# Kernel optimization log

Hardware: AMD Instinct MI355X
Metric: run time of the kernel (lower is better)

Reference implementation:

```python
import jax, jax.numpy as jnp
import numpy as np

N_NODES = 100000
N_EDGES = 1600000
NODE_DIM = 128
EDGE_DIM = 64
MSG_DIM = 128
NODE_DIM_OUT = 128


def setup_inputs() -> dict:
    key = jax.random.key(0)
    k1, k2, k3, k4, k5, k6, k7 = jax.random.split(key, 7)
    node_emb = jax.random.normal(k1, (N_NODES, NODE_DIM), dtype=jnp.float32)
    edge_index = jax.random.randint(k2, (2, N_EDGES), 0, N_NODES, dtype=jnp.int64)
    edge_emb = jax.random.normal(k3, (N_EDGES, EDGE_DIM), dtype=jnp.float32)
    # Linear params (stored as [in, out]; torch uses [out, in] with x @ W.T)
    s_msg = 1.0 / np.sqrt(NODE_DIM + EDGE_DIM)
    W_msg = jax.random.uniform(k4, (NODE_DIM + EDGE_DIM, MSG_DIM), jnp.float32, -s_msg, s_msg)
    b_msg = jax.random.uniform(k5, (MSG_DIM,), jnp.float32, -s_msg, s_msg)
    s_upd = 1.0 / np.sqrt(NODE_DIM + MSG_DIM)
    W_upd = jax.random.uniform(k6, (NODE_DIM + MSG_DIM, NODE_DIM_OUT), jnp.float32, -s_upd, s_upd)
    b_upd = jax.random.uniform(k7, (NODE_DIM_OUT,), jnp.float32, -s_upd, s_upd)
    return {"node_emb": node_emb, "edge_index": edge_index, "edge_emb": edge_emb,
            "W_msg": W_msg, "b_msg": b_msg, "W_upd": W_upd, "b_upd": b_upd}


def reference(node_emb, edge_index, edge_emb, W_msg, b_msg, W_upd, b_upd):
    # PyG MessagePassing default flow: x_j = x[edge_index[0]] (source),
    # messages aggregated (mean) at edge_index[1] (target).
    src = edge_index[0]
    dst = edge_index[1]
    n = node_emb.shape[0]

    x_j = node_emb[src]                                    # [E, node_dim] gather
    msg_in = jnp.concatenate([x_j, edge_emb], axis=1)      # [E, node_dim+edge_dim]
    msg = jax.nn.relu(msg_in @ W_msg + b_msg)              # [E, msg_dim]

    # scatter-mean aggregate to nodes
    summed = jax.ops.segment_sum(msg, dst, num_segments=n)  # [N, msg_dim]
    counts = jax.ops.segment_sum(jnp.ones((msg.shape[0],), dtype=msg.dtype), dst, num_segments=n)
    mean_msg = summed / jnp.maximum(counts, 1.0)[:, None]

    upd_in = jnp.concatenate([node_emb, mean_msg], axis=1)  # [N, node_dim+msg_dim]
    h = jax.nn.relu(upd_in @ W_upd + b_upd)                 # [N, node_dim_out]
    # dropout is identity in eval mode; normalize=False (default)
    return h
```

## Files before the change

kernel.cpp:

```cpp
#include <hip/hip_runtime.h>
#include <hip/hip_bf16.h>

#define N_NODES 100000
#define N_EDGES 1600000
#define D_NODE 128
#define D_EDGE 64
#define D_MSG 128
#define K1 192
#define K2 256
#define D_OUT 128
#define NSB 98
#define TILE 64
#define NT (N_EDGES / TILE)

using frag8 = __attribute__((ext_vector_type(8))) short;
using facc  = __attribute__((ext_vector_type(4))) float;

static __device__ __forceinline__ unsigned short f2bf(float f) {
    unsigned int u = __float_as_uint(f);
    u = u + 0x7fffu + ((u >> 16) & 1u);
    return (unsigned short)(u >> 16);
}
static __device__ __forceinline__ float bflo(unsigned int u) { return __uint_as_float(u << 16); }
static __device__ __forceinline__ float bfhi(unsigned int u) { return __uint_as_float(u & 0xffff0000u); }

union F8 { unsigned short s[8]; frag8 f; uint4 u4; };

static __device__ __forceinline__ frag8 pack8(float4 a, float4 b) {
    F8 u;
    u.s[0] = f2bf(a.x); u.s[1] = f2bf(a.y); u.s[2] = f2bf(a.z); u.s[3] = f2bf(a.w);
    u.s[4] = f2bf(b.x); u.s[5] = f2bf(b.y); u.s[6] = f2bf(b.z); u.s[7] = f2bf(b.w);
    return u.f;
}

__global__ void prep_w_kernel(const float* __restrict__ Wm, const float* __restrict__ Wu,
                              unsigned short* __restrict__ WtM, unsigned short* __restrict__ WtU) {
    int idx0 = blockIdx.x * blockDim.x + threadIdx.x;
    int stride = gridDim.x * blockDim.x;
    for (int idx = idx0; idx < 128 * K1; idx += stride) {
        int o = idx / K1, k = idx - o * K1;
        WtM[idx] = f2bf(Wm[k * D_MSG + o]);
    }
    for (int idx = idx0; idx < 128 * K2; idx += stride) {
        int o = idx >> 8, k = idx & 255;
        WtU[idx] = f2bf(Wu[k * D_OUT + o]);
    }
}

__global__ void prep_node_kernel(const float* __restrict__ node_emb,
                                 unsigned int* __restrict__ nodeB32) {
    int idx0 = blockIdx.x * blockDim.x + threadIdx.x;
    int stride = gridDim.x * blockDim.x;
    const int total = N_NODES * 64;
    for (int i = idx0; i < total; i += stride) {
        float2 v = *(const float2*)&node_emb[(size_t)i * 2];
        nodeB32[i] = (unsigned)f2bf(v.x) | ((unsigned)f2bf(v.y) << 16);
    }
}

__global__ void hist_kernel(const int* __restrict__ dst, int* __restrict__ cnt) {
    int idx0 = blockIdx.x * blockDim.x + threadIdx.x;
    int stride = gridDim.x * blockDim.x;
    for (int e = idx0; e < N_EDGES; e += stride) {
        int d = min(max(dst[e], 0), N_NODES - 1);
        atomicAdd(&cnt[d], 1);
    }
}

__global__ __launch_bounds__(1024) void scan_blocks(const int* __restrict__ cnt,
                                                    int* __restrict__ base,
                                                    int* __restrict__ part) {
    __shared__ int sh[1024];
    int i = blockIdx.x * 1024 + threadIdx.x;
    int c = (i < N_NODES) ? cnt[i] : 0;
    sh[threadIdx.x] = c;
    __syncthreads();
    for (int s = 1; s < 1024; s <<= 1) {
        int t = (threadIdx.x >= s) ? sh[threadIdx.x - s] : 0;
        __syncthreads();
        sh[threadIdx.x] += t;
        __syncthreads();
    }
    if (i < N_NODES) base[i] = sh[threadIdx.x] - c;
    if (threadIdx.x == 1023) part[blockIdx.x] = sh[1023];
}

__global__ __launch_bounds__(128) void scan_partials(int* __restrict__ part) {
    __shared__ int sh[128];
    int i = threadIdx.x;
    int c = (i < NSB) ? part[i] : 0;
    sh[i] = c;
    __syncthreads();
    for (int s = 1; s < 128; s <<= 1) {
        int t = (i >= s) ? sh[i - s] : 0;
        __syncthreads();
        sh[i] += t;
        __syncthreads();
    }
    if (i < NSB) part[i] = sh[i] - c;
}

__global__ __launch_bounds__(1024) void scan_add(int* __restrict__ base, const int* __restrict__ part) {
    int i = blockIdx.x * 1024 + threadIdx.x;
    if (i < N_NODES) base[i] += part[blockIdx.x];
}

__global__ void scatter_kernel(const int* __restrict__ dst, const int* __restrict__ src,
                               const int* __restrict__ base, int* __restrict__ cursor,
                               int* __restrict__ perm, int* __restrict__ srcS,
                               int* __restrict__ dstS) {
    int idx0 = blockIdx.x * blockDim.x + threadIdx.x;
    int stride = gridDim.x * blockDim.x;
    for (int e = idx0; e < N_EDGES; e += stride) {
        int d = min(max(dst[e], 0), N_NODES - 1);
        int pos = base[d] + atomicAdd(&cursor[d], 1);
        perm[pos] = e;
        srcS[pos] = src[e];
        dstS[pos] = d;
    }
}

__global__ __launch_bounds__(256, 3) void msg_fused_kernel(
    const unsigned short* __restrict__ nodeB, const int* __restrict__ srcS,
    const int* __restrict__ perm, const int* __restrict__ dstS,
    const float* __restrict__ edge_emb, const unsigned short* __restrict__ WtM,
    const float* __restrict__ b_msg, const int* __restrict__ base,
    const int* __restrict__ cnt, float* __restrict__ mean)
{
    __shared__ unsigned short sIn[TILE][192];
    __shared__ unsigned short sMsg[TILE][128];

    const int lane = threadIdx.x & 63;
    const int wav  = threadIdx.x >> 6;
    const int j = lane & 15;
    const int q = lane >> 4;

    frag8 wfr[2][6];
#pragma unroll
    for (int m2 = 0; m2 < 2; ++m2) {
        const unsigned short* wrow = WtM + ((wav * 2 + m2) * 16 + j) * K1;
#pragma unroll
        for (int kc = 0; kc < 6; ++kc)
            wfr[m2][kc] = *(const frag8*)&wrow[(kc * 4 + q) * 8];
    }
    float bias[2][4];
#pragma unroll
    for (int m2 = 0; m2 < 2; ++m2)
#pragma unroll
        for (int r = 0; r < 4; ++r) bias[m2][r] = b_msg[(wav * 2 + m2) * 16 + q * 4 + r];

    const int eL = threadIdx.x >> 2;
    const int qt = threadIdx.x & 3;
    const int swz = eL & 7;

    uint4  nst[4];
    float4 est[4];

    const int t0 = blockIdx.x;

    {
        const int e = t0 * TILE + eL;
        const int sp = min(max(srcS[e], 0), N_NODES - 1);
        const unsigned short* nrow = nodeB + (size_t)sp * D_NODE + qt * 32;
#pragma unroll
        for (int i = 0; i < 4; ++i) nst[i] = *(const uint4*)&nrow[i * 8];
        const float* erow = edge_emb + (size_t)perm[e] * D_EDGE + qt * 16;
#pragma unroll
        for (int i = 0; i < 4; ++i) est[i] = *(const float4*)&erow[i * 4];
    }

#pragma unroll 1
    for (int t = t0; t < NT; t += gridDim.x) {
        const int e0 = t * TILE;

        __syncthreads();

        {
            unsigned short* drow = &sIn[eL][0];
#pragma unroll
            for (int i = 0; i < 4; ++i)
                *(uint4*)&drow[((4 * qt + i) ^ swz) * 8] = nst[i];
#pragma unroll
            for (int h = 0; h < 2; ++h) {
                F8 u;
                u.f = pack8(est[h * 2], est[h * 2 + 1]);
                *(uint4*)&drow[((16 + 2 * qt + h) ^ swz) * 8] = u.u4;
            }
        }
        __syncthreads();

        const int tn = t + gridDim.x;
        if (tn < NT) {
            const int e = tn * TILE + eL;
            const int sp = min(max(srcS[e], 0), N_NODES - 1);
            const unsigned short* nrow = nodeB + (size_t)sp * D_NODE + qt * 32;
#pragma unroll
            for (int i = 0; i < 4; ++i) nst[i] = *(const uint4*)&nrow[i * 8];
            const float* erow = edge_emb + (size_t)perm[e] * D_EDGE + qt * 16;
#pragma unroll
            for (int i = 0; i < 4; ++i) est[i] = *(const float4*)&erow[i * 4];
        }

        facc acc[2][4];
#pragma unroll
        for (int m2 = 0; m2 < 2; ++m2)
#pragma unroll
            for (int eg = 0; eg < 4; ++eg) { facc z = {0.f,0.f,0.f,0.f}; acc[m2][eg] = z; }

        const int rsw = j & 7;
#pragma unroll
        for (int eg = 0; eg < 4; ++eg) {
            const unsigned short* irow = &sIn[eg * 16 + j][0];
#pragma unroll
            for (int kc = 0; kc < 6; ++kc) {
                frag8 b = *(const frag8*)&irow[((4 * kc + q) ^ rsw) * 8];
                acc[0][eg] = __builtin_amdgcn_mfma_f32_16x16x32_bf16(wfr[0][kc], b, acc[0][eg], 0, 0, 0);
                acc[1][eg] = __builtin_amdgcn_mfma_f32_16x16x32_bf16(wfr[1][kc], b, acc[1][eg], 0, 0, 0);
            }
        }

#pragma unroll
        for (int eg = 0; eg < 4; ++eg) {
            unsigned short* mrow = &sMsg[eg * 16 + j][0];
#pragma unroll
            for (int m2 = 0; m2 < 2; ++m2) {
                float v0 = fmaxf(acc[m2][eg][0] + bias[m2][0], 0.f);
                float v1 = fmaxf(acc[m2][eg][1] + bias[m2][1], 0.f);
                float v2 = fmaxf(acc[m2][eg][2] + bias[m2][2], 0.f);
                float v3 = fmaxf(acc[m2][eg][3] + bias[m2][3], 0.f);
                uint2 w;
                w.x = (unsigned)f2bf(v0) | ((unsigned)f2bf(v1) << 16);
                w.y = (unsigned)f2bf(v2) | ((unsigned)f2bf(v3) << 16);
                int c64 = wav * 8 + m2 * 4 + q;
                *(uint2*)&mrow[(c64 ^ rsw) * 4] = w;
            }
        }
        __syncthreads();

        const int d_lo = dstS[e0];
        const int d_hi = dstS[e0 + TILE - 1];
        for (int n = d_lo + wav; n <= d_hi; n += 4) {
            const int b = base[n];
            const int c = cnt[n];
            const int lo = max(b - e0, 0);
            const int hi = min(b + c - e0, TILE);
            float s0 = 0.f, s1 = 0.f;
            for (int r = lo; r < hi; ++r) {
                const unsigned* mr = (const unsigned*)&sMsg[r][0];
                unsigned u = mr[(((lane >> 1) ^ (r & 7)) << 1) | (lane & 1)];
                s0 += bflo(u); s1 += bfhi(u);
            }
            const float inv = 1.0f / fmaxf((float)c, 1.0f);
            s0 *= inv; s1 *= inv;
            float* mp = mean + (size_t)n * D_MSG + lane * 2;
            if (b >= e0 && b + c <= e0 + TILE) {
                *(float2*)mp = make_float2(s0, s1);
            } else {
                atomicAdd(mp + 0, s0);
                atomicAdd(mp + 1, s1);
            }
        }
    }
}

__global__ __launch_bounds__(256) void node_gemm_kernel(
    const unsigned short* __restrict__ nodeB, const float* __restrict__ mean,
    const unsigned short* __restrict__ WtU, const float* __restrict__ b_upd,
    float* __restrict__ out)
{
    __shared__ unsigned short sW[128 * K2];

    for (int idx = threadIdx.x; idx < 128 * 32; idx += 256) {
        int o = idx >> 5, ch = idx & 31;
        *(uint4*)&sW[o * K2 + (ch ^ (o & 7)) * 8] = *(const uint4*)&WtU[o * K2 + ch * 8];
    }

    const int lane = threadIdx.x & 63;
    const int wav  = threadIdx.x >> 6;
    const int j = lane & 15;
    const int q = lane >> 4;
    const int rs = j & 7;

    float bias[32];
#pragma unroll
    for (int mt = 0; mt < 8; ++mt)
#pragma unroll
        for (int r = 0; r < 4; ++r) bias[mt * 4 + r] = b_upd[mt * 16 + q * 4 + r];
    __syncthreads();

    const int n0w = blockIdx.x * 256 + wav * 64;

#pragma unroll 1
    for (int g = 0; g < 4; ++g) {
        const int n = n0w + g * 16 + j;
        const bool valid = (n < N_NODES);
        const size_t nn = valid ? (size_t)n : 0;

        frag8 bfr[8];
        const unsigned short* nrow = nodeB + nn * D_NODE;
#pragma unroll
        for (int kc = 0; kc < 4; ++kc)
            bfr[kc] = *(const frag8*)&nrow[kc * 32 + q * 8];
        const float* mrow = mean + nn * D_MSG;
#pragma unroll
        for (int kc = 0; kc < 4; ++kc) {
            float4 a = *(const float4*)&mrow[kc * 32 + q * 8];
            float4 c = *(const float4*)&mrow[kc * 32 + q * 8 + 4];
            bfr[4 + kc] = pack8(a, c);
        }

        facc acc[8];
#pragma unroll
        for (int mt = 0; mt < 8; ++mt) { facc z = {0.f, 0.f, 0.f, 0.f}; acc[mt] = z; }

#pragma unroll
        for (int mt = 0; mt < 8; ++mt) {
            const unsigned short* wrow = &sW[(mt * 16 + j) * K2];
#pragma unroll
            for (int kc = 0; kc < 8; ++kc) {
                frag8 a = *(const frag8*)&wrow[((kc * 4 + q) ^ rs) * 8];
                acc[mt] = __builtin_amdgcn_mfma_f32_16x16x32_bf16(a, bfr[kc], acc[mt], 0, 0, 0);
            }
        }

        if (valid) {
            float* orow = out + (size_t)n * D_OUT;
#pragma unroll
            for (int mt = 0; mt < 8; ++mt)
#pragma unroll
                for (int r = 0; r < 4; ++r)
                    orow[mt * 16 + q * 4 + r] = fmaxf(acc[mt][r] + bias[mt * 4 + r], 0.f);
        }
    }
}

__global__ __launch_bounds__(256) void msg_agg_kernel_fb(
    const float* __restrict__ node_emb, const int* __restrict__ src,
    const float* __restrict__ edge_emb, const unsigned short* __restrict__ WtM,
    const float* __restrict__ b_msg, const int* __restrict__ perm,
    const int* __restrict__ dstS, const int* __restrict__ cnt,
    float* __restrict__ mean)
{
    __shared__ unsigned short sW[128 * K1];

    for (int idx = threadIdx.x; idx < 128 * 24; idx += 256) {
        int o = idx / 24, ch = idx % 24;
        *(uint4*)&sW[o * K1 + (ch ^ (o & 7)) * 8] = *(const uint4*)&WtM[o * K1 + ch * 8];
    }

    const int lane = threadIdx.x & 63;
    const int wav  = threadIdx.x >> 6;
    const int j = lane & 15;
    const int q = lane >> 4;

    float bias[32];
#pragma unroll
    for (int mt = 0; mt < 8; ++mt)
#pragma unroll
        for (int r = 0; r < 4; ++r) bias[mt * 4 + r] = b_msg[mt * 16 + q * 4 + r];
    __syncthreads();

    const int e0w = blockIdx.x * 256 + wav * 64;
    float carry[32];
    int carry_d = -1;

#pragma unroll 1
    for (int g = 0; g < 4; ++g) {
        const int e = e0w + g * 16 + j;
        const int p = perm[e];
        const int d = dstS[e];
        const int sp = min(max(src[p], 0), N_NODES - 1);
        const float invc = 1.0f / (float)cnt[d];

        frag8 bfr[6];
        const float* nrow = node_emb + (size_t)sp * D_NODE;
#pragma unroll
        for (int kc = 0; kc < 4; ++kc) {
            float4 a = *(const float4*)&nrow[kc * 32 + q * 8];
            float4 c = *(const float4*)&nrow[kc * 32 + q * 8 + 4];
            bfr[kc] = pack8(a, c);
        }
        const float* erow = edge_emb + (size_t)p * D_EDGE;
#pragma unroll
        for (int kc = 0; kc < 2; ++kc) {
            float4 a = *(const float4*)&erow[kc * 32 + q * 8];
            float4 c = *(const float4*)&erow[kc * 32 + q * 8 + 4];
            bfr[4 + kc] = pack8(a, c);
        }

        facc acc[8];
#pragma unroll
        for (int mt = 0; mt < 8; ++mt) { facc z = {0.f, 0.f, 0.f, 0.f}; acc[mt] = z; }

#pragma unroll
        for (int mt = 0; mt < 8; ++mt) {
            const unsigned short* wrow = &sW[(mt * 16 + j) * K1];
            const int rs = j & 7;
#pragma unroll
            for (int kc = 0; kc < 6; ++kc) {
                frag8 a = *(const frag8*)&wrow[((kc * 4 + q) ^ rs) * 8];
                acc[mt] = __builtin_amdgcn_mfma_f32_16x16x32_bf16(a, bfr[kc], acc[mt], 0, 0, 0);
            }
        }

        float v[32];
#pragma unroll
        for (int mt = 0; mt < 8; ++mt)
#pragma unroll
            for (int r = 0; r < 4; ++r) {
                float t = acc[mt][r] + bias[mt * 4 + r];
                v[mt * 4 + r] = fmaxf(t, 0.f) * invc;
            }

        int dprev = __shfl_up(d, 1, 16);
        int head = (j == 0 || d != dprev) ? 1 : 0;
        int seg = head;
#pragma unroll
        for (int s = 1; s < 16; s <<= 1) { int t = __shfl_up(seg, s, 16); if (j >= s) seg += t; }
        int sg1 = __shfl_up(seg, 1, 16);
        int sg2 = __shfl_up(seg, 2, 16);
        int sg4 = __shfl_up(seg, 4, 16);
        int sg8 = __shfl_up(seg, 8, 16);
        bool ok1 = (j >= 1) && (sg1 == seg);
        bool ok2 = (j >= 2) && (sg2 == seg);
        bool ok4 = (j >= 4) && (sg4 == seg);
        bool ok8 = (j >= 8) && (sg8 == seg);

#pragma unroll
        for (int i = 0; i < 32; ++i) { float t = __shfl_up(v[i], 1, 16); if (ok1) v[i] += t; }
#pragma unroll
        for (int i = 0; i < 32; ++i) { float t = __shfl_up(v[i], 2, 16); if (ok2) v[i] += t; }
#pragma unroll
        for (int i = 0; i < 32; ++i) { float t = __shfl_up(v[i], 4, 16); if (ok4) v[i] += t; }
#pragma unroll
        for (int i = 0; i < 32; ++i) { float t = __shfl_up(v[i], 8, 16); if (ok8) v[i] += t; }

        int d0 = __shfl(d, 0, 16);
        if (g > 0) {
            if (d0 != carry_d) {
                if (j == 0) {
                    float* mrow = mean + (size_t)carry_d * D_MSG;
#pragma unroll
                    for (int mt = 0; mt < 8; ++mt)
#pragma unroll
                        for (int r = 0; r < 4; ++r)
                            atomicAdd(&mrow[mt * 16 + q * 4 + r], carry[mt * 4 + r]);
                }
            } else if (seg == 1) {
#pragma unroll
                for (int i = 0; i < 32; ++i) v[i] += carry[i];
            }
        }

#pragma unroll
        for (int i = 0; i < 32; ++i) carry[i] = __shfl(v[i], 15, 16);
        carry_d = __shfl(d, 15, 16);

        int dnext = __shfl_down(d, 1, 16);
        bool tail = (j < 15) ? (dnext != d) : (g == 3);
        if (tail) {
            float* mrow = mean + (size_t)d * D_MSG;
#pragma unroll
            for (int mt = 0; mt < 8; ++mt)
#pragma unroll
                for (int r = 0; r < 4; ++r)
                    atomicAdd(&mrow[mt * 16 + q * 4 + r], v[mt * 4 + r]);
        }
    }
}

__global__ __launch_bounds__(256) void node_kernel_fb(
    const float* __restrict__ node_emb, const float* __restrict__ mean,
    const unsigned short* __restrict__ WtU, const float* __restrict__ b_upd,
    float* __restrict__ out)
{
    __shared__ unsigned short sW[128 * K2];

    for (int idx = threadIdx.x; idx < 128 * 32; idx += 256) {
        int o = idx >> 5, ch = idx & 31;
        *(uint4*)&sW[o * K2 + (ch ^ (o & 7)) * 8] = *(const uint4*)&WtU[o * K2 + ch * 8];
    }

    const int lane = threadIdx.x & 63;
    const int wav  = threadIdx.x >> 6;
    const int j = lane & 15;
    const int q = lane >> 4;

    float bias[32];
#pragma unroll
    for (int mt = 0; mt < 8; ++mt)
#pragma unroll
        for (int r = 0; r < 4; ++r) bias[mt * 4 + r] = b_upd[mt * 16 + q * 4 + r];
    __syncthreads();

    const int n0w = blockIdx.x * 256 + wav * 64;

#pragma unroll 1
    for (int g = 0; g < 4; ++g) {
        const int n = n0w + g * 16 + j;
        const bool valid = (n < N_NODES);
        const size_t nn = valid ? (size_t)n : 0;

        frag8 bfr[8];
        const float* nrow = node_emb + nn * D_NODE;
#pragma unroll
        for (int kc = 0; kc < 4; ++kc) {
            float4 a = *(const float4*)&nrow[kc * 32 + q * 8];
            float4 c = *(const float4*)&nrow[kc * 32 + q * 8 + 4];
            bfr[kc] = pack8(a, c);
        }
        const float* mrow = mean + nn * D_MSG;
#pragma unroll
        for (int kc = 0; kc < 4; ++kc) {
            float4 a = *(const float4*)&mrow[kc * 32 + q * 8];
            float4 c = *(const float4*)&mrow[kc * 32 + q * 8 + 4];
            bfr[4 + kc] = pack8(a, c);
        }

        facc acc[8];
#pragma unroll
        for (int mt = 0; mt < 8; ++mt) { facc z = {0.f, 0.f, 0.f, 0.f}; acc[mt] = z; }

#pragma unroll
        for (int mt = 0; mt < 8; ++mt) {
            const unsigned short* wrow = &sW[(mt * 16 + j) * K2];
            const int rs = j & 7;
#pragma unroll
            for (int kc = 0; kc < 8; ++kc) {
                frag8 a = *(const frag8*)&wrow[((kc * 4 + q) ^ rs) * 8];
                acc[mt] = __builtin_amdgcn_mfma_f32_16x16x32_bf16(a, bfr[kc], acc[mt], 0, 0, 0);
            }
        }

        if (valid) {
            float* orow = out + (size_t)n * D_OUT;
#pragma unroll
            for (int mt = 0; mt < 8; ++mt)
#pragma unroll
                for (int r = 0; r < 4; ++r)
                    orow[mt * 16 + q * 4 + r] = fmaxf(acc[mt][r] + bias[mt * 4 + r], 0.f);
        }
    }
}

extern "C" void kernel_launch(void* const* d_in, const int* in_sizes, int n_in,
                              void* d_out, int out_size, void* d_ws, size_t ws_size,
                              hipStream_t stream) {
    const float* node_emb = (const float*)d_in[0];
    const int*   edge_idx = (const int*)d_in[1];
    const float* edge_emb = (const float*)d_in[2];
    const float* W_msg    = (const float*)d_in[3];
    const float* b_msg    = (const float*)d_in[4];
    const float* W_upd    = (const float*)d_in[5];
    const float* b_upd    = (const float*)d_in[6];
    float* out = (float*)d_out;

    const int* src = edge_idx;
    const int* dst = edge_idx + N_EDGES;

    char* W = (char*)d_ws;

    if (ws_size >= 97315200ULL) {
        float* mean  = (float*)(W + 0);
        int* cnt     = (int*)(W + 51200000);
        int* cursor  = (int*)(W + 51600000);
        int* base    = (int*)(W + 52000000);
        int* part    = (int*)(W + 52400000);
        int* perm    = (int*)(W + 52400512);
        int* srcS    = (int*)(W + 58800512);
        int* dstS    = (int*)(W + 65200512);
        unsigned short* WtM   = (unsigned short*)(W + 71600512);
        unsigned short* WtU   = (unsigned short*)(W + 71649664);
        unsigned short* nodeB = (unsigned short*)(W + 71715200);

        hipMemsetAsync(d_ws, 0, 52000000, stream);

        prep_w_kernel<<<224, 256, 0, stream>>>(W_msg, W_upd, WtM, WtU);
        prep_node_kernel<<<2048, 256, 0, stream>>>(node_emb, (unsigned int*)nodeB);
        hist_kernel<<<1024, 256, 0, stream>>>(dst, cnt);
        scan_blocks<<<NSB, 1024, 0, stream>>>(cnt, base, part);
        scan_partials<<<1, 128, 0, stream>>>(part);
        scan_add<<<NSB, 1024, 0, stream>>>(base, part);
        scatter_kernel<<<1024, 256, 0, stream>>>(dst, src, base, cursor, perm, srcS, dstS);
        msg_fused_kernel<<<2048, 256, 0, stream>>>(nodeB, srcS, perm, dstS, edge_emb,
                                                   WtM, b_msg, base, cnt, mean);
        node_gemm_kernel<<<391, 256, 0, stream>>>(nodeB, mean, WtU, b_upd, out);
    } else {
        float* mean  = (float*)W;
        int* cnt     = (int*)(W + 51200000);
        int* cursor  = (int*)(W + 51600000);
        int* base    = (int*)(W + 52000000);
        int* part    = (int*)(W + 52400000);
        int* perm    = (int*)(W + 52400512);
        int* dstS    = (int*)(W + 58800512);
        int* srcS    = (int*)(W + 65200512);
        unsigned short* WtM = (unsigned short*)(W + 71600512);
        unsigned short* WtU = (unsigned short*)(W + 71649664);

        hipMemsetAsync(d_ws, 0, 52000000, stream);

        prep_w_kernel<<<224, 256, 0, stream>>>(W_msg, W_upd, WtM, WtU);
        hist_kernel<<<1024, 256, 0, stream>>>(dst, cnt);
        scan_blocks<<<NSB, 1024, 0, stream>>>(cnt, base, part);
        scan_partials<<<1, 128, 0, stream>>>(part);
        scan_add<<<NSB, 1024, 0, stream>>>(base, part);
        scatter_kernel<<<1024, 256, 0, stream>>>(dst, src, base, cursor, perm, srcS, dstS);
        msg_agg_kernel_fb<<<6250, 256, 0, stream>>>(node_emb, src, edge_emb, WtM,
                                                    b_msg, perm, dstS, cnt, mean);
        node_kernel_fb<<<391, 256, 0, stream>>>(node_emb, mean, WtU, b_upd, out);
    }
}
```

Before: 604.9 us.

## Pre-sort edge embeddings to bf16, replace boundary atomics with spill+cleanup pass

The scatter pass now writes edge embeddings converted to bf16 in destination-sorted order, so the message kernel reads them contiguously at half the size instead of gathering fp32 rows through perm. Partial sums for nodes that straddle tile boundaries go to a per-tile spill buffer, and a new cleanup kernel reduces them into mean instead of using float atomics. This lets the large memset of mean be dropped. The weight, node-conversion and histogram prep kernels are merged into one launch, and the message kernel's occupancy hint rises from 3 to 4. In exchange the scatter pass writes roughly 200MB more, and the workspace requirement grows a lot, so a smaller workspace falls back to the slower path.

```diff
diff --git a/kernel.cpp b/kernel.cpp
--- a/kernel.cpp
+++ b/kernel.cpp
@@ -33,8 +33,10 @@
     return u.f;
 }
 
-__global__ void prep_w_kernel(const float* __restrict__ Wm, const float* __restrict__ Wu,
-                              unsigned short* __restrict__ WtM, unsigned short* __restrict__ WtU) {
+__global__ void prep_all_kernel(const float* __restrict__ Wm, const float* __restrict__ Wu,
+                                const float* __restrict__ node_emb, const int* __restrict__ dst,
+                                unsigned short* __restrict__ WtM, unsigned short* __restrict__ WtU,
+                                unsigned int* __restrict__ nodeB32, int* __restrict__ cnt) {
     int idx0 = blockIdx.x * blockDim.x + threadIdx.x;
     int stride = gridDim.x * blockDim.x;
     for (int idx = idx0; idx < 128 * K1; idx += stride) {
@@ -45,22 +47,11 @@
         int o = idx >> 8, k = idx & 255;
         WtU[idx] = f2bf(Wu[k * D_OUT + o]);
     }
-}
-
-__global__ void prep_node_kernel(const float* __restrict__ node_emb,
-                                 unsigned int* __restrict__ nodeB32) {
-    int idx0 = blockIdx.x * blockDim.x + threadIdx.x;
-    int stride = gridDim.x * blockDim.x;
     const int total = N_NODES * 64;
     for (int i = idx0; i < total; i += stride) {
         float2 v = *(const float2*)&node_emb[(size_t)i * 2];
         nodeB32[i] = (unsigned)f2bf(v.x) | ((unsigned)f2bf(v.y) << 16);
     }
-}
-
-__global__ void hist_kernel(const int* __restrict__ dst, int* __restrict__ cnt) {
-    int idx0 = blockIdx.x * blockDim.x + threadIdx.x;
-    int stride = gridDim.x * blockDim.x;
     for (int e = idx0; e < N_EDGES; e += stride) {
         int d = min(max(dst[e], 0), N_NODES - 1);
         atomicAdd(&cnt[d], 1);
@@ -105,6 +96,290 @@
     if (i < N_NODES) base[i] += part[blockIdx.x];
 }
 
+__global__ void scatter2_kernel(const int* __restrict__ dst, const int* __restrict__ src,
+                                const float* __restrict__ edge_emb,
+                                const int* __restrict__ base, int* __restrict__ cursor,
+                                int* __restrict__ srcS, int* __restrict__ dstS,
+                                unsigned short* __restrict__ edgeB) {
+    int idx0 = blockIdx.x * blockDim.x + threadIdx.x;
+    int stride = gridDim.x * blockDim.x;
+    for (int e = idx0; e < N_EDGES; e += stride) {
+        int d = min(max(dst[e], 0), N_NODES - 1);
+        int pos = base[d] + atomicAdd(&cursor[d], 1);
+        srcS[pos] = src[e];
+        dstS[pos] = d;
+        const float* er = edge_emb + (size_t)e * D_EDGE;
+        unsigned short* ob = edgeB + (size_t)pos * D_EDGE;
+#pragma unroll
+        for (int c = 0; c < 4; ++c) {
+            float4 a = *(const float4*)&er[c * 16 + 0];
+            float4 b = *(const float4*)&er[c * 16 + 4];
+            float4 g = *(const float4*)&er[c * 16 + 8];
+            float4 h = *(const float4*)&er[c * 16 + 12];
+            F8 u0; u0.f = pack8(a, b);
+            F8 u1; u1.f = pack8(g, h);
+            *(uint4*)&ob[c * 16 + 0] = u0.u4;
+            *(uint4*)&ob[c * 16 + 8] = u1.u4;
+        }
+    }
+}
+
+__global__ __launch_bounds__(256, 4) void msg_fused_kernel(
+    const unsigned short* __restrict__ nodeB, const int* __restrict__ srcS,
+    const int* __restrict__ dstS, const unsigned short* __restrict__ edgeB,
+    const unsigned short* __restrict__ WtM, const float* __restrict__ b_msg,
+    const int* __restrict__ base, const int* __restrict__ cnt,
+    float* __restrict__ mean, float* __restrict__ spill)
+{
+    __shared__ unsigned short sIn[TILE][192];
+    __shared__ unsigned short sMsg[TILE][128];
+
+    const int lane = threadIdx.x & 63;
+    const int wav  = threadIdx.x >> 6;
+    const int j = lane & 15;
+    const int q = lane >> 4;
+
+    frag8 wfr[2][6];
+#pragma unroll
+    for (int m2 = 0; m2 < 2; ++m2) {
+        const unsigned short* wrow = WtM + ((wav * 2 + m2) * 16 + j) * K1;
+#pragma unroll
+        for (int kc = 0; kc < 6; ++kc)
+            wfr[m2][kc] = *(const frag8*)&wrow[(kc * 4 + q) * 8];
+    }
+    float bias[2][4];
+#pragma unroll
+    for (int m2 = 0; m2 < 2; ++m2)
+#pragma unroll
+        for (int r = 0; r < 4; ++r) bias[m2][r] = b_msg[(wav * 2 + m2) * 16 + q * 4 + r];
+
+    const int eL = threadIdx.x >> 2;
+    const int qt = threadIdx.x & 3;
+    const int swz = eL & 7;
+
+    uint4 nst[4];
+    uint4 est[2];
+
+    const int t0 = blockIdx.x;
+
+    {
+        const int e = t0 * TILE + eL;
+        const int sp = min(max(srcS[e], 0), N_NODES - 1);
+        const unsigned short* nrow = nodeB + (size_t)sp * D_NODE + qt * 32;
+#pragma unroll
+        for (int i = 0; i < 4; ++i) nst[i] = *(const uint4*)&nrow[i * 8];
+        const unsigned short* erow = edgeB + (size_t)e * D_EDGE + qt * 16;
+        est[0] = *(const uint4*)&erow[0];
+        est[1] = *(const uint4*)&erow[8];
+    }
+
+#pragma unroll 1
+    for (int t = t0; t < NT; t += gridDim.x) {
+        const int e0 = t * TILE;
+
+        __syncthreads();
+
+        {
+            unsigned short* drow = &sIn[eL][0];
+#pragma unroll
+            for (int i = 0; i < 4; ++i)
+                *(uint4*)&drow[((4 * qt + i) ^ swz) * 8] = nst[i];
+#pragma unroll
+            for (int h = 0; h < 2; ++h)
+                *(uint4*)&drow[((16 + 2 * qt + h) ^ swz) * 8] = est[h];
+        }
+        __syncthreads();
+
+        const int tn = t + gridDim.x;
+        if (tn < NT) {
+            const int e = tn * TILE + eL;
+            const int sp = min(max(srcS[e], 0), N_NODES - 1);
+            const unsigned short* nrow = nodeB + (size_t)sp * D_NODE + qt * 32;
+#pragma unroll
+            for (int i = 0; i < 4; ++i) nst[i] = *(const uint4*)&nrow[i * 8];
+            const unsigned short* erow = edgeB + (size_t)e * D_EDGE + qt * 16;
+            est[0] = *(const uint4*)&erow[0];
+            est[1] = *(const uint4*)&erow[8];
+        }
+
+        facc acc[2][4];
+#pragma unroll
+        for (int m2 = 0; m2 < 2; ++m2)
+#pragma unroll
+            for (int eg = 0; eg < 4; ++eg) { facc z = {0.f,0.f,0.f,0.f}; acc[m2][eg] = z; }
+
+        const int rsw = j & 7;
+#pragma unroll
+        for (int eg = 0; eg < 4; ++eg) {
+            const unsigned short* irow = &sIn[eg * 16 + j][0];
+#pragma unroll
+            for (int kc = 0; kc < 6; ++kc) {
+                frag8 b = *(const frag8*)&irow[((4 * kc + q) ^ rsw) * 8];
+                acc[0][eg] = __builtin_amdgcn_mfma_f32_16x16x32_bf16(wfr[0][kc], b, acc[0][eg], 0, 0, 0);
+                acc[1][eg] = __builtin_amdgcn_mfma_f32_16x16x32_bf16(wfr[1][kc], b, acc[1][eg], 0, 0, 0);
+            }
+        }
+
+#pragma unroll
+        for (int eg = 0; eg < 4; ++eg) {
+            unsigned short* mrow = &sMsg[eg * 16 + j][0];
+#pragma unroll
+            for (int m2 = 0; m2 < 2; ++m2) {
+                float v0 = fmaxf(acc[m2][eg][0] + bias[m2][0], 0.f);
+                float v1 = fmaxf(acc[m2][eg][1] + bias[m2][1], 0.f);
+                float v2 = fmaxf(acc[m2][eg][2] + bias[m2][2], 0.f);
+                float v3 = fmaxf(acc[m2][eg][3] + bias[m2][3], 0.f);
+                uint2 w;
+                w.x = (unsigned)f2bf(v0) | ((unsigned)f2bf(v1) << 16);
+                w.y = (unsigned)f2bf(v2) | ((unsigned)f2bf(v3) << 16);
+                int c64 = wav * 8 + m2 * 4 + q;
+                *(uint2*)&mrow[(c64 ^ rsw) * 4] = w;
+            }
+        }
+        __syncthreads();
+
+        const int d_lo = dstS[e0];
+        const int d_hi = dstS[e0 + TILE - 1];
+        for (int n = d_lo + wav; n <= d_hi; n += 4) {
+            const int b = base[n];
+            const int c = cnt[n];
+            const int lo = max(b - e0, 0);
+            const int hi = min(b + c - e0, TILE);
+            float s0 = 0.f, s1 = 0.f;
+            for (int r = lo; r < hi; ++r) {
+                const unsigned* mr = (const unsigned*)&sMsg[r][0];
+                unsigned u = mr[(((lane >> 1) ^ (r & 7)) << 1) | (lane & 1)];
+                s0 += bflo(u); s1 += bfhi(u);
+            }
+            const float inv = 1.0f / fmaxf((float)c, 1.0f);
+            s0 *= inv; s1 *= inv;
+            if (b >= e0 && b + c <= e0 + TILE) {
+                *(float2*)(mean + (size_t)n * D_MSG + lane * 2) = make_float2(s0, s1);
+            } else {
+                int slot = (n == d_lo) ? 0 : 1;
+                *(float2*)(spill + ((size_t)(t * 2 + slot)) * D_MSG + lane * 2) = make_float2(s0, s1);
+            }
+        }
+    }
+}
+
+__global__ __launch_bounds__(256) void cleanup_kernel(
+    const int* __restrict__ dstS, const int* __restrict__ base,
+    const int* __restrict__ cnt, const float* __restrict__ spill,
+    float* __restrict__ mean)
+{
+    const int wav = threadIdx.x >> 6;
+    const int lane = threadIdx.x & 63;
+    const int n = blockIdx.x * 4 + wav;
+    const int c = cnt[n];
+    float s0 = 0.f, s1 = 0.f;
+    if (c > 0) {
+        const int b = base[n];
+        const int t0 = b >> 6, t1 = (b + c - 1) >> 6;
+        if (t0 == t1) return;
+        for (int t = t0; t <= t1; ++t) {
+            const int slot = (dstS[t * TILE] == n) ? 0 : 1;
+            const float* sp = spill + ((size_t)(t * 2 + slot)) * D_MSG + lane * 2;
+            s0 += sp[0]; s1 += sp[1];
+        }
+    }
+    *(float2*)(mean + (size_t)n * D_MSG + lane * 2) = make_float2(s0, s1);
+}
+
+__global__ __launch_bounds__(256) void node_gemm_kernel(
+    const unsigned short* __restrict__ nodeB, const float* __restrict__ mean,
+    const unsigned short* __restrict__ WtU, const float* __restrict__ b_upd,
+    float* __restrict__ out)
+{
+    __shared__ unsigned short sW[128 * K2];
+
+    for (int idx = threadIdx.x; idx < 128 * 32; idx += 256) {
+        int o = idx >> 5, ch = idx & 31;
+        *(uint4*)&sW[o * K2 + (ch ^ (o & 7)) * 8] = *(const uint4*)&WtU[o * K2 + ch * 8];
+    }
+
+    const int lane = threadIdx.x & 63;
+    const int wav  = threadIdx.x >> 6;
+    const int j = lane & 15;
+    const int q = lane >> 4;
+    const int rs = j & 7;
+
+    float bias[32];
+#pragma unroll
+    for (int mt = 0; mt < 8; ++mt)
+#pragma unroll
+        for (int r = 0; r < 4; ++r) bias[mt * 4 + r] = b_upd[mt * 16 + q * 4 + r];
+    __syncthreads();
+
+    const int n0w = blockIdx.x * 256 + wav * 64;
+
+#pragma unroll 1
+    for (int g = 0; g < 4; ++g) {
+        const int n = n0w + g * 16 + j;
+        const bool valid = (n < N_NODES);
+        const size_t nn = valid ? (size_t)n : 0;
+
+        frag8 bfr[8];
+        const unsigned short* nrow = nodeB + nn * D_NODE;
+#pragma unroll
+        for (int kc = 0; kc < 4; ++kc)
+            bfr[kc] = *(const frag8*)&nrow[kc * 32 + q * 8];
+        const float* mrow = mean + nn * D_MSG;
+#pragma unroll
+        for (int kc = 0; kc < 4; ++kc) {
+            float4 a = *(const float4*)&mrow[kc * 32 + q * 8];
+            float4 c = *(const float4*)&mrow[kc * 32 + q * 8 + 4];
+            bfr[4 + kc] = pack8(a, c);
+        }
+
+        facc acc[8];
+#pragma unroll
+        for (int mt = 0; mt < 8; ++mt) { facc z = {0.f, 0.f, 0.f, 0.f}; acc[mt] = z; }
+
+#pragma unroll
+        for (int mt = 0; mt < 8; ++mt) {
+            const unsigned short* wrow = &sW[(mt * 16 + j) * K2];
+#pragma unroll
+            for (int kc = 0; kc < 8; ++kc) {
+                frag8 a = *(const frag8*)&wrow[((kc * 4 + q) ^ rs) * 8];
+                acc[mt] = __builtin_amdgcn_mfma_f32_16x16x32_bf16(a, bfr[kc], acc[mt], 0, 0, 0);
+            }
+        }
+
+        if (valid) {
+            float* orow = out + (size_t)n * D_OUT;
+#pragma unroll
+            for (int mt = 0; mt < 8; ++mt)
+#pragma unroll
+                for (int r = 0; r < 4; ++r)
+                    orow[mt * 16 + q * 4 + r] = fmaxf(acc[mt][r] + bias[mt * 4 + r], 0.f);
+        }
+    }
+}
+
+__global__ void prep_w_kernel(const float* __restrict__ Wm, const float* __restrict__ Wu,
+                              unsigned short* __restrict__ WtM, unsigned short* __restrict__ WtU) {
+    int idx0 = blockIdx.x * blockDim.x + threadIdx.x;
+    int stride = gridDim.x * blockDim.x;
+    for (int idx = idx0; idx < 128 * K1; idx += stride) {
+        int o = idx / K1, k = idx - o * K1;
+        WtM[idx] = f2bf(Wm[k * D_MSG + o]);
+    }
+    for (int idx = idx0; idx < 128 * K2; idx += stride) {
+        int o = idx >> 8, k = idx & 255;
+        WtU[idx] = f2bf(Wu[k * D_OUT + o]);
+    }
+}
+
+__global__ void hist_kernel(const int* __restrict__ dst, int* __restrict__ cnt) {
+    int idx0 = blockIdx.x * blockDim.x + threadIdx.x;
+    int stride = gridDim.x * blockDim.x;
+    for (int e = idx0; e < N_EDGES; e += stride) {
+        int d = min(max(dst[e], 0), N_NODES - 1);
+        atomicAdd(&cnt[d], 1);
+    }
+}
+
 __global__ void scatter_kernel(const int* __restrict__ dst, const int* __restrict__ src,
                                const int* __restrict__ base, int* __restrict__ cursor,
                                int* __restrict__ perm, int* __restrict__ srcS,
@@ -120,220 +395,6 @@
     }
 }
 
-__global__ __launch_bounds__(256, 3) void msg_fused_kernel(
-    const unsigned short* __restrict__ nodeB, const int* __restrict__ srcS,
-    const int* __restrict__ perm, const int* __restrict__ dstS,
-    const float* __restrict__ edge_emb, const unsigned short* __restrict__ WtM,
-    const float* __restrict__ b_msg, const int* __restrict__ base,
-    const int* __restrict__ cnt, float* __restrict__ mean)
-{
-    __shared__ unsigned short sIn[TILE][192];
-    __shared__ unsigned short sMsg[TILE][128];
-
-    const int lane = threadIdx.x & 63;
-    const int wav  = threadIdx.x >> 6;
-    const int j = lane & 15;
-    const int q = lane >> 4;
-
-    frag8 wfr[2][6];
-#pragma unroll
-    for (int m2 = 0; m2 < 2; ++m2) {
-        const unsigned short* wrow = WtM + ((wav * 2 + m2) * 16 + j) * K1;
-#pragma unroll
-        for (int kc = 0; kc < 6; ++kc)
-            wfr[m2][kc] = *(const frag8*)&wrow[(kc * 4 + q) * 8];
-    }
-    float bias[2][4];
-#pragma unroll
-    for (int m2 = 0; m2 < 2; ++m2)
-#pragma unroll
-        for (int r = 0; r < 4; ++r) bias[m2][r] = b_msg[(wav * 2 + m2) * 16 + q * 4 + r];
-
-    const int eL = threadIdx.x >> 2;
-    const int qt = threadIdx.x & 3;
-    const int swz = eL & 7;
-
-    uint4  nst[4];
-    float4 est[4];
-
-    const int t0 = blockIdx.x;
-
-    {
-        const int e = t0 * TILE + eL;
-        const int sp = min(max(srcS[e], 0), N_NODES - 1);
-        const unsigned short* nrow = nodeB + (size_t)sp * D_NODE + qt * 32;
-#pragma unroll
-        for (int i = 0; i < 4; ++i) nst[i] = *(const uint4*)&nrow[i * 8];
-        const float* erow = edge_emb + (size_t)perm[e] * D_EDGE + qt * 16;
-#pragma unroll
-        for (int i = 0; i < 4; ++i) est[i] = *(const float4*)&erow[i * 4];
-    }
-
-#pragma unroll 1
-    for (int t = t0; t < NT; t += gridDim.x) {
-        const int e0 = t * TILE;
-
-        __syncthreads();
-
-        {
-            unsigned short* drow = &sIn[eL][0];
-#pragma unroll
-            for (int i = 0; i < 4; ++i)
-                *(uint4*)&drow[((4 * qt + i) ^ swz) * 8] = nst[i];
-#pragma unroll
-            for (int h = 0; h < 2; ++h) {
-                F8 u;
-                u.f = pack8(est[h * 2], est[h * 2 + 1]);
-                *(uint4*)&drow[((16 + 2 * qt + h) ^ swz) * 8] = u.u4;
-            }
-        }
-        __syncthreads();
-
-        const int tn = t + gridDim.x;
-        if (tn < NT) {
-            const int e = tn * TILE + eL;
-            const int sp = min(max(srcS[e], 0), N_NODES - 1);
-            const unsigned short* nrow = nodeB + (size_t)sp * D_NODE + qt * 32;
-#pragma unroll
-            for (int i = 0; i < 4; ++i) nst[i] = *(const uint4*)&nrow[i * 8];
-            const float* erow = edge_emb + (size_t)perm[e] * D_EDGE + qt * 16;
-#pragma unroll
-            for (int i = 0; i < 4; ++i) est[i] = *(const float4*)&erow[i * 4];
-        }
-
-        facc acc[2][4];
-#pragma unroll
-        for (int m2 = 0; m2 < 2; ++m2)
-#pragma unroll
-            for (int eg = 0; eg < 4; ++eg) { facc z = {0.f,0.f,0.f,0.f}; acc[m2][eg] = z; }
-
-        const int rsw = j & 7;
-#pragma unroll
-        for (int eg = 0; eg < 4; ++eg) {
-            const unsigned short* irow = &sIn[eg * 16 + j][0];
-#pragma unroll
-            for (int kc = 0; kc < 6; ++kc) {
-                frag8 b = *(const frag8*)&irow[((4 * kc + q) ^ rsw) * 8];
-                acc[0][eg] = __builtin_amdgcn_mfma_f32_16x16x32_bf16(wfr[0][kc], b, acc[0][eg], 0, 0, 0);
-                acc[1][eg] = __builtin_amdgcn_mfma_f32_16x16x32_bf16(wfr[1][kc], b, acc[1][eg], 0, 0, 0);
-            }
-        }
-
-#pragma unroll
-        for (int eg = 0; eg < 4; ++eg) {
-            unsigned short* mrow = &sMsg[eg * 16 + j][0];
-#pragma unroll
-            for (int m2 = 0; m2 < 2; ++m2) {
-                float v0 = fmaxf(acc[m2][eg][0] + bias[m2][0], 0.f);
-                float v1 = fmaxf(acc[m2][eg][1] + bias[m2][1], 0.f);
-                float v2 = fmaxf(acc[m2][eg][2] + bias[m2][2], 0.f);
-                float v3 = fmaxf(acc[m2][eg][3] + bias[m2][3], 0.f);
-                uint2 w;
-                w.x = (unsigned)f2bf(v0) | ((unsigned)f2bf(v1) << 16);
-                w.y = (unsigned)f2bf(v2) | ((unsigned)f2bf(v3) << 16);
-                int c64 = wav * 8 + m2 * 4 + q;
-                *(uint2*)&mrow[(c64 ^ rsw) * 4] = w;
-            }
-        }
-        __syncthreads();
-
-        const int d_lo = dstS[e0];
-        const int d_hi = dstS[e0 + TILE - 1];
-        for (int n = d_lo + wav; n <= d_hi; n += 4) {
-            const int b = base[n];
-            const int c = cnt[n];
-            const int lo = max(b - e0, 0);
-            const int hi = min(b + c - e0, TILE);
-            float s0 = 0.f, s1 = 0.f;
-            for (int r = lo; r < hi; ++r) {
-                const unsigned* mr = (const unsigned*)&sMsg[r][0];
-                unsigned u = mr[(((lane >> 1) ^ (r & 7)) << 1) | (lane & 1)];
-                s0 += bflo(u); s1 += bfhi(u);
-            }
-            const float inv = 1.0f / fmaxf((float)c, 1.0f);
-            s0 *= inv; s1 *= inv;
-            float* mp = mean + (size_t)n * D_MSG + lane * 2;
-            if (b >= e0 && b + c <= e0 + TILE) {
-                *(float2*)mp = make_float2(s0, s1);
-            } else {
-                atomicAdd(mp + 0, s0);
-                atomicAdd(mp + 1, s1);
-            }
-        }
-    }
-}
-
-__global__ __launch_bounds__(256) void node_gemm_kernel(
-    const unsigned short* __restrict__ nodeB, const float* __restrict__ mean,
-    const unsigned short* __restrict__ WtU, const float* __restrict__ b_upd,
-    float* __restrict__ out)
-{
-    __shared__ unsigned short sW[128 * K2];
-
-    for (int idx = threadIdx.x; idx < 128 * 32; idx += 256) {
-        int o = idx >> 5, ch = idx & 31;
-        *(uint4*)&sW[o * K2 + (ch ^ (o & 7)) * 8] = *(const uint4*)&WtU[o * K2 + ch * 8];
-    }
-
-    const int lane = threadIdx.x & 63;
-    const int wav  = threadIdx.x >> 6;
-    const int j = lane & 15;
-    const int q = lane >> 4;
-    const int rs = j & 7;
-
-    float bias[32];
-#pragma unroll
-    for (int mt = 0; mt < 8; ++mt)
-#pragma unroll
-        for (int r = 0; r < 4; ++r) bias[mt * 4 + r] = b_upd[mt * 16 + q * 4 + r];
-    __syncthreads();
-
-    const int n0w = blockIdx.x * 256 + wav * 64;
-
-#pragma unroll 1
-    for (int g = 0; g < 4; ++g) {
-        const int n = n0w + g * 16 + j;
-        const bool valid = (n < N_NODES);
-        const size_t nn = valid ? (size_t)n : 0;
-
-        frag8 bfr[8];
-        const unsigned short* nrow = nodeB + nn * D_NODE;
-#pragma unroll
-        for (int kc = 0; kc < 4; ++kc)
-            bfr[kc] = *(const frag8*)&nrow[kc * 32 + q * 8];
-        const float* mrow = mean + nn * D_MSG;
-#pragma unroll
-        for (int kc = 0; kc < 4; ++kc) {
-            float4 a = *(const float4*)&mrow[kc * 32 + q * 8];
-            float4 c = *(const float4*)&mrow[kc * 32 + q * 8 + 4];
-            bfr[4 + kc] = pack8(a, c);
-        }
-
-        facc acc[8];
-#pragma unroll
-        for (int mt = 0; mt < 8; ++mt) { facc z = {0.f, 0.f, 0.f, 0.f}; acc[mt] = z; }
-
-#pragma unroll
-        for (int mt = 0; mt < 8; ++mt) {
-            const unsigned short* wrow = &sW[(mt * 16 + j) * K2];
-#pragma unroll
-            for (int kc = 0; kc < 8; ++kc) {
-                frag8 a = *(const frag8*)&wrow[((kc * 4 + q) ^ rs) * 8];
-                acc[mt] = __builtin_amdgcn_mfma_f32_16x16x32_bf16(a, bfr[kc], acc[mt], 0, 0, 0);
-            }
-        }
-
-        if (valid) {
-            float* orow = out + (size_t)n * D_OUT;
-#pragma unroll
-            for (int mt = 0; mt < 8; ++mt)
-#pragma unroll
-                for (int r = 0; r < 4; ++r)
-                    orow[mt * 16 + q * 4 + r] = fmaxf(acc[mt][r] + bias[mt * 4 + r], 0.f);
-        }
-    }
-}
-
 __global__ __launch_bounds__(256) void msg_agg_kernel_fb(
     const float* __restrict__ node_emb, const int* __restrict__ src,
     const float* __restrict__ edge_emb, const unsigned short* __restrict__ WtM,
@@ -560,30 +621,32 @@
 
     char* W = (char*)d_ws;
 
-    if (ws_size >= 97315200ULL) {
+    if (ws_size >= 321315200ULL) {
         float* mean  = (float*)(W + 0);
         int* cnt     = (int*)(W + 51200000);
         int* cursor  = (int*)(W + 51600000);
         int* base    = (int*)(W + 52000000);
         int* part    = (int*)(W + 52400000);
-        int* perm    = (int*)(W + 52400512);
-        int* srcS    = (int*)(W + 58800512);
-        int* dstS    = (int*)(W + 65200512);
-        unsigned short* WtM   = (unsigned short*)(W + 71600512);
-        unsigned short* WtU   = (unsigned short*)(W + 71649664);
-        unsigned short* nodeB = (unsigned short*)(W + 71715200);
-
-        hipMemsetAsync(d_ws, 0, 52000000, stream);
-
-        prep_w_kernel<<<224, 256, 0, stream>>>(W_msg, W_upd, WtM, WtU);
-        prep_node_kernel<<<2048, 256, 0, stream>>>(node_emb, (unsigned int*)nodeB);
-        hist_kernel<<<1024, 256, 0, stream>>>(dst, cnt);
+        int* srcS    = (int*)(W + 52400512);
+        int* dstS    = (int*)(W + 58800512);
+        unsigned short* WtM   = (unsigned short*)(W + 65200512);
+        unsigned short* WtU   = (unsigned short*)(W + 65249664);
+        unsigned short* nodeB = (unsigned short*)(W + 65315200);
+        unsigned short* edgeB = (unsigned short*)(W + 90915200);
+        float* spill = (float*)(W + 295715200);
+
+        hipMemsetAsync(W + 51200000, 0, 800000, stream);
+
+        prep_all_kernel<<<2048, 256, 0, stream>>>(W_msg, W_upd, node_emb, dst,
+                                                  WtM, WtU, (unsigned int*)nodeB, cnt);
         scan_blocks<<<NSB, 1024, 0, stream>>>(cnt, base, part);
         scan_partials<<<1, 128, 0, stream>>>(part);
         scan_add<<<NSB, 1024, 0, stream>>>(base, part);
-        scatter_kernel<<<1024, 256, 0, stream>>>(dst, src, base, cursor, perm, srcS, dstS);
-        msg_fused_kernel<<<2048, 256, 0, stream>>>(nodeB, srcS, perm, dstS, edge_emb,
-                                                   WtM, b_msg, base, cnt, mean);
+        scatter2_kernel<<<2048, 256, 0, stream>>>(dst, src, edge_emb, base, cursor,
+                                                  srcS, dstS, edgeB);
+        msg_fused_kernel<<<2048, 256, 0, stream>>>(nodeB, srcS, dstS, edgeB,
+                                                   WtM, b_msg, base, cnt, mean, spill);
+        cleanup_kernel<<<25000, 256, 0, stream>>>(dstS, base, cnt, spill, mean);
         node_gemm_kernel<<<391, 256, 0, stream>>>(nodeB, mean, WtU, b_upd, out);
     } else {
         float* mean  = (float*)W;
```

New measurement: 715.4 us. +18.3%, slower.

## Store mean in bf16, replace boundary atomics with spill slots and cleanup pass

Applied to the files above, without the earlier changes.

The mean buffer is now stored as packed bf16 instead of fp32, which halves its size and lets the big workspace memset shrink to just the counters. Messages for nodes that straddle a tile boundary are written to per-tile spill slots, and a new cleanup kernel sums them instead of using float atomics. The three prep kernels are merged into one launch, and msg_fused occupancy is raised to 4 waves per SIMD. The trade-off is an extra kernel launch, lower mean precision, and register pressure from the tighter launch bound.

```diff
diff --git a/kernel.cpp b/kernel.cpp
--- a/kernel.cpp
+++ b/kernel.cpp
@@ -33,8 +33,10 @@
     return u.f;
 }
 
-__global__ void prep_w_kernel(const float* __restrict__ Wm, const float* __restrict__ Wu,
-                              unsigned short* __restrict__ WtM, unsigned short* __restrict__ WtU) {
+__global__ void prep_all_kernel(const float* __restrict__ Wm, const float* __restrict__ Wu,
+                                const float* __restrict__ node_emb, const int* __restrict__ dst,
+                                unsigned short* __restrict__ WtM, unsigned short* __restrict__ WtU,
+                                unsigned int* __restrict__ nodeB32, int* __restrict__ cnt) {
     int idx0 = blockIdx.x * blockDim.x + threadIdx.x;
     int stride = gridDim.x * blockDim.x;
     for (int idx = idx0; idx < 128 * K1; idx += stride) {
@@ -45,22 +47,11 @@
         int o = idx >> 8, k = idx & 255;
         WtU[idx] = f2bf(Wu[k * D_OUT + o]);
     }
-}
-
-__global__ void prep_node_kernel(const float* __restrict__ node_emb,
-                                 unsigned int* __restrict__ nodeB32) {
-    int idx0 = blockIdx.x * blockDim.x + threadIdx.x;
-    int stride = gridDim.x * blockDim.x;
     const int total = N_NODES * 64;
     for (int i = idx0; i < total; i += stride) {
         float2 v = *(const float2*)&node_emb[(size_t)i * 2];
         nodeB32[i] = (unsigned)f2bf(v.x) | ((unsigned)f2bf(v.y) << 16);
     }
-}
-
-__global__ void hist_kernel(const int* __restrict__ dst, int* __restrict__ cnt) {
-    int idx0 = blockIdx.x * blockDim.x + threadIdx.x;
-    int stride = gridDim.x * blockDim.x;
     for (int e = idx0; e < N_EDGES; e += stride) {
         int d = min(max(dst[e], 0), N_NODES - 1);
         atomicAdd(&cnt[d], 1);
@@ -120,12 +111,13 @@
     }
 }
 
-__global__ __launch_bounds__(256, 3) void msg_fused_kernel(
+__global__ __launch_bounds__(256, 4) void msg_fused_kernel(
     const unsigned short* __restrict__ nodeB, const int* __restrict__ srcS,
     const int* __restrict__ perm, const int* __restrict__ dstS,
     const float* __restrict__ edge_emb, const unsigned short* __restrict__ WtM,
     const float* __restrict__ b_msg, const int* __restrict__ base,
-    const int* __restrict__ cnt, float* __restrict__ mean)
+    const int* __restrict__ cnt, unsigned int* __restrict__ meanB32,
+    float* __restrict__ spill)
 {
     __shared__ unsigned short sIn[TILE][192];
     __shared__ unsigned short sMsg[TILE][128];
@@ -252,19 +244,43 @@
             }
             const float inv = 1.0f / fmaxf((float)c, 1.0f);
             s0 *= inv; s1 *= inv;
-            float* mp = mean + (size_t)n * D_MSG + lane * 2;
             if (b >= e0 && b + c <= e0 + TILE) {
-                *(float2*)mp = make_float2(s0, s1);
+                meanB32[(size_t)n * 64 + lane] =
+                    (unsigned)f2bf(s0) | ((unsigned)f2bf(s1) << 16);
             } else {
-                atomicAdd(mp + 0, s0);
-                atomicAdd(mp + 1, s1);
-            }
-        }
-    }
+                int slot = (n == d_lo) ? 0 : 1;
+                *(float2*)(spill + ((size_t)(t * 2 + slot)) * D_MSG + lane * 2) =
+                    make_float2(s0, s1);
+            }
+        }
+    }
+}
+
+__global__ __launch_bounds__(256) void cleanup_kernel(
+    const int* __restrict__ dstS, const int* __restrict__ base,
+    const int* __restrict__ cnt, const float* __restrict__ spill,
+    unsigned int* __restrict__ meanB32)
+{
+    const int wav = threadIdx.x >> 6;
+    const int lane = threadIdx.x & 63;
+    const int n = blockIdx.x * 4 + wav;
+    const int c = cnt[n];
+    float s0 = 0.f, s1 = 0.f;
+    if (c > 0) {
+        const int b = base[n];
+        const int t0 = b >> 6, t1 = (b + c - 1) >> 6;
+        if (t0 == t1) return;
+        for (int t = t0; t <= t1; ++t) {
+            const int slot = (dstS[t * TILE] == n) ? 0 : 1;
+            const float* sp = spill + ((size_t)(t * 2 + slot)) * D_MSG + lane * 2;
+            s0 += sp[0]; s1 += sp[1];
+        }
+    }
+    meanB32[(size_t)n * 64 + lane] = (unsigned)f2bf(s0) | ((unsigned)f2bf(s1) << 16);
 }
 
 __global__ __launch_bounds__(256) void node_gemm_kernel(
-    const unsigned short* __restrict__ nodeB, const float* __restrict__ mean,
+    const unsigned short* __restrict__ nodeB, const unsigned short* __restrict__ meanB,
     const unsigned short* __restrict__ WtU, const float* __restrict__ b_upd,
     float* __restrict__ out)
 {
@@ -301,13 +317,10 @@
 #pragma unroll
         for (int kc = 0; kc < 4; ++kc)
             bfr[kc] = *(const frag8*)&nrow[kc * 32 + q * 8];
-        const float* mrow = mean + nn * D_MSG;
-#pragma unroll
-        for (int kc = 0; kc < 4; ++kc) {
-            float4 a = *(const float4*)&mrow[kc * 32 + q * 8];
-            float4 c = *(const float4*)&mrow[kc * 32 + q * 8 + 4];
-            bfr[4 + kc] = pack8(a, c);
-        }
+        const unsigned short* mrow = meanB + nn * D_MSG;
+#pragma unroll
+        for (int kc = 0; kc < 4; ++kc)
+            bfr[4 + kc] = *(const frag8*)&mrow[kc * 32 + q * 8];
 
         facc acc[8];
 #pragma unroll
@@ -331,6 +344,29 @@
                 for (int r = 0; r < 4; ++r)
                     orow[mt * 16 + q * 4 + r] = fmaxf(acc[mt][r] + bias[mt * 4 + r], 0.f);
         }
+    }
+}
+
+__global__ void prep_w_kernel(const float* __restrict__ Wm, const float* __restrict__ Wu,
+                              unsigned short* __restrict__ WtM, unsigned short* __restrict__ WtU) {
+    int idx0 = blockIdx.x * blockDim.x + threadIdx.x;
+    int stride = gridDim.x * blockDim.x;
+    for (int idx = idx0; idx < 128 * K1; idx += stride) {
+        int o = idx / K1, k = idx - o * K1;
+        WtM[idx] = f2bf(Wm[k * D_MSG + o]);
+    }
+    for (int idx = idx0; idx < 128 * K2; idx += stride) {
+        int o = idx >> 8, k = idx & 255;
+        WtU[idx] = f2bf(Wu[k * D_OUT + o]);
+    }
+}
+
+__global__ void hist_kernel(const int* __restrict__ dst, int* __restrict__ cnt) {
+    int idx0 = blockIdx.x * blockDim.x + threadIdx.x;
+    int stride = gridDim.x * blockDim.x;
+    for (int e = idx0; e < N_EDGES; e += stride) {
+        int d = min(max(dst[e], 0), N_NODES - 1);
+        atomicAdd(&cnt[d], 1);
     }
 }
 
@@ -560,31 +596,34 @@
 
     char* W = (char*)d_ws;
 
-    if (ws_size >= 97315200ULL) {
-        float* mean  = (float*)(W + 0);
-        int* cnt     = (int*)(W + 51200000);
-        int* cursor  = (int*)(W + 51600000);
-        int* base    = (int*)(W + 52000000);
-        int* part    = (int*)(W + 52400000);
-        int* perm    = (int*)(W + 52400512);
-        int* srcS    = (int*)(W + 58800512);
-        int* dstS    = (int*)(W + 65200512);
-        unsigned short* WtM   = (unsigned short*)(W + 71600512);
-        unsigned short* WtU   = (unsigned short*)(W + 71649664);
-        unsigned short* nodeB = (unsigned short*)(W + 71715200);
-
-        hipMemsetAsync(d_ws, 0, 52000000, stream);
-
-        prep_w_kernel<<<224, 256, 0, stream>>>(W_msg, W_upd, WtM, WtU);
-        prep_node_kernel<<<2048, 256, 0, stream>>>(node_emb, (unsigned int*)nodeB);
-        hist_kernel<<<1024, 256, 0, stream>>>(dst, cnt);
+    if (ws_size >= 98000000ULL) {
+        unsigned short* meanB = (unsigned short*)(W + 0);
+        int* cnt     = (int*)(W + 25600000);
+        int* cursor  = (int*)(W + 26000000);
+        int* base    = (int*)(W + 26400000);
+        int* part    = (int*)(W + 26800000);
+        int* perm    = (int*)(W + 26800512);
+        int* srcS    = (int*)(W + 33200512);
+        int* dstS    = (int*)(W + 39600512);
+        unsigned short* WtM   = (unsigned short*)(W + 46000512);
+        unsigned short* WtU   = (unsigned short*)(W + 46049664);
+        unsigned short* nodeB = (unsigned short*)(W + 46115200);
+        float* spill = (float*)(W + 71715200);
+
+        hipMemsetAsync(W + 25600000, 0, 800000, stream);
+
+        prep_all_kernel<<<2048, 256, 0, stream>>>(W_msg, W_upd, node_emb, dst,
+                                                  WtM, WtU, (unsigned int*)nodeB, cnt);
         scan_blocks<<<NSB, 1024, 0, stream>>>(cnt, base, part);
         scan_partials<<<1, 128, 0, stream>>>(part);
         scan_add<<<NSB, 1024, 0, stream>>>(base, part);
         scatter_kernel<<<1024, 256, 0, stream>>>(dst, src, base, cursor, perm, srcS, dstS);
         msg_fused_kernel<<<2048, 256, 0, stream>>>(nodeB, srcS, perm, dstS, edge_emb,
-                                                   WtM, b_msg, base, cnt, mean);
-        node_gemm_kernel<<<391, 256, 0, stream>>>(nodeB, mean, WtU, b_upd, out);
+                                                   WtM, b_msg, base, cnt,
+                                                   (unsigned int*)meanB, spill);
+        cleanup_kernel<<<25000, 256, 0, stream>>>(dstS, base, cnt, spill,
+                                                  (unsigned int*)meanB);
+        node_gemm_kernel<<<391, 256, 0, stream>>>(nodeB, meanB, WtU, b_upd, out);
     } else {
         float* mean  = (float*)W;
         int* cnt     = (int*)(W + 51200000);
```

Measured after the change: 611.1 us. No clear change (+1.0%).
